# Kernel tuning notes

Hardware: AMD Instinct MI355X
Metric: run time of the kernel (lower is better)

The kernel has to match this reference:

```python
import jax, jax.numpy as jnp
import numpy as np


def setup_inputs() -> dict:
    key = jax.random.key(0)
    k1, k2, k3, k4, k5 = jax.random.split(key, 5)
    B, L, D = 8, 4096, 64
    return {
        "Q": jax.random.normal(k1, (B, L, D), dtype=jnp.float32),
        "K": jax.random.normal(k2, (B, L, D), dtype=jnp.float32),
        "V": jax.random.normal(k3, (B, L, D), dtype=jnp.float32),
        "sent_embed_slice": jax.random.normal(k4, (B, D), dtype=jnp.float32),
        "proj": jax.random.normal(k5, (D, D), dtype=jnp.float32),  # fixed phi projection (M, d)
        "qkv_size": 64,
        "masked": 1,
    }


def _phi(X, proj, M):
    # X: (B, L, d). Original applies phi per timestep slice x = X[:, t, :] of shape (B, d)
    # phi(x) = (1/sqrt(M)) * exp(-0.5 * ||x||_F) * exp(proj @ x), Frobenius norm over the (B, d) slice.
    logits = jnp.einsum("bld,md->blm", X, proj)            # (B, L, M)
    scale = jnp.exp(-0.5 * jnp.sqrt(jnp.sum(X * X, axis=(0, 2))))  # per-timestep scalar, (L,)
    return jnp.exp(logits) * scale[None, :, None] / jnp.sqrt(jnp.asarray(M, jnp.float32))


def reference(Q, K, V, sent_embed_slice, proj, qkv_size, masked):
    M = qkv_size
    phi_q = _phi(Q, proj, M)  # (B, L, M)
    phi_k = _phi(K, proj, M)  # (B, L, M)
    if masked:
        # causal running sums: KV_t = sum_{j<=t} phi_k_j outer V_j ; N_t = sum_{j<=t} phi_k_j
        KV = jnp.cumsum(phi_k[:, :, :, None] * V[:, :, None, :], axis=1)  # (B, L, M, D)
        Nc = jnp.cumsum(phi_k, axis=1)                                    # (B, L, M)
        num = jnp.einsum("blm,blmd->bld", phi_q, KV)
        r = jnp.einsum("blm,blm->bl", phi_q, Nc)
        return num / (r + jnp.sign(r) * 1e-6)[:, :, None]
    else:
        KV = jnp.einsum("blm,bld->bmd", phi_k, V)     # (B, M, D)
        Ns = jnp.sum(phi_k, axis=1)                    # (B, M); broadcast over D like torch norm_sum
        num = jnp.einsum("blm,bmd->bld", phi_q, KV)
        r = jnp.einsum("blm,bm->bl", phi_q, Ns)
        return num / r[:, :, None]
```

## Files before the change

kernel.cpp:

```cpp
#include <hip/hip_runtime.h>
#include <math.h>

#define BB 8
#define LL 4096
#define DD 64
#define SS 64
#define NCHUNK 64
#define STATE 4160

typedef __attribute__((ext_vector_type(8))) short s16x8;
typedef __attribute__((ext_vector_type(8))) unsigned short u16x8;
typedef __attribute__((ext_vector_type(4))) float f32x4;

#define MFMA(a, b, c) __builtin_amdgcn_mfma_f32_16x16x32_bf16((a), (b), (c), 0, 0, 0)

static __device__ __forceinline__ unsigned short f2bf(float x) {
  unsigned int u = __builtin_bit_cast(unsigned int, x);
  u += 0x7FFFu + ((u >> 16) & 1u);
  return (unsigned short)(u >> 16);
}
static __device__ __forceinline__ float bf2f(unsigned short h) {
  unsigned int u = ((unsigned int)h) << 16;
  return __builtin_bit_cast(float, u);
}

static __device__ __forceinline__ s16x8 ld_frag(const unsigned short* base, int row0, int ks) {
  const int lane = threadIdx.x & 63;
  const int r = row0 + (lane & 15);
  const int idx = r * 64 + ((ks * 32 + ((lane & 48) >> 1)) ^ ((r & 7) << 3));
  return *(const s16x8*)(base + idx);
}

static __device__ __forceinline__ void stage_hl(unsigned short* __restrict__ Sh,
                                                unsigned short* __restrict__ Sl,
                                                const float* __restrict__ src, int tid) {
#pragma unroll
  for (int it = 0; it < 2; ++it) {
    const int g = tid + it * 256;
    const int row = g >> 3;
    const int c0 = (g & 7) * 8;
    const float4 x0 = *(const float4*)(src + row * 64 + c0);
    const float4 x1 = *(const float4*)(src + row * 64 + c0 + 4);
    const float xs[8] = {x0.x, x0.y, x0.z, x0.w, x1.x, x1.y, x1.z, x1.w};
    u16x8 h, l;
#pragma unroll
    for (int k = 0; k < 8; ++k) {
      const unsigned short hh = f2bf(xs[k]);
      h[k] = hh;
      l[k] = f2bf(xs[k] - bf2f(hh));
    }
    const int idx = row * 64 + (c0 ^ ((row & 7) << 3));
    *(u16x8*)(Sh + idx) = h;
    *(u16x8*)(Sl + idx) = l;
  }
}

static __device__ __forceinline__ void stage_vfull(float* __restrict__ F, const float* __restrict__ src,
                                                   int tid) {
#pragma unroll
  for (int it = 0; it < 4; ++it) {
    const int g = tid + it * 256;
    const int row = g >> 4;
    const int col = (g & 15) * 4;
    *(float4*)(F + row * 64 + col) = *(const float4*)(src + row * 64 + col);
  }
}

static __device__ __forceinline__ void stage_img(unsigned short* __restrict__ S,
                                                 const unsigned short* __restrict__ src, int tid) {
#pragma unroll
  for (int it = 0; it < 2; ++it) {
    const int g = tid + it * 256;
    const int row = g >> 3;
    const int c0 = (g & 7) * 8;
    *(u16x8*)(S + row * 64 + (c0 ^ ((row & 7) << 3))) = *(const u16x8*)(src + row * 64 + c0);
  }
}

static __device__ __forceinline__ void vtrans_half(unsigned short* __restrict__ Gh,
                                                   unsigned short* __restrict__ Hl,
                                                   const float* __restrict__ F, int tid, int half) {
  const int d = tid & 63;
  const int tb = (tid >> 6) * 8;
  float v[8];
#pragma unroll
  for (int k = 0; k < 8; ++k) v[k] = F[(tb + k) * 64 + d];
  u16x8 hh, ll;
#pragma unroll
  for (int k = 0; k < 8; ++k) {
    const unsigned short h = f2bf(v[k]);
    hh[k] = h;
    ll[k] = f2bf(v[k] - bf2f(h));
  }
  const int idx = d * 64 + ((half * 32 + tb) ^ ((d & 7) << 3));
  *(u16x8*)(Gh + idx) = hh;
  *(u16x8*)(Hl + idx) = ll;
}

static __device__ __forceinline__ void logits3(const unsigned short* Ah_, const unsigned short* Al_,
                                               const unsigned short* Bh_, const unsigned short* Bl_,
                                               int w, f32x4 acc[4]) {
  s16x8 ah[2], al[2];
#pragma unroll
  for (int ks = 0; ks < 2; ++ks) {
    ah[ks] = ld_frag(Ah_, w * 16, ks);
    al[ks] = ld_frag(Al_, w * 16, ks);
  }
#pragma unroll
  for (int ct = 0; ct < 4; ++ct) {
#pragma unroll
    for (int ks = 0; ks < 2; ++ks) {
      const s16x8 bh = ld_frag(Bh_, ct * 16, ks);
      const s16x8 bl = ld_frag(Bl_, ct * 16, ks);
      acc[ct] = MFMA(ah[ks], bh, acc[ct]);
      acc[ct] = MFMA(ah[ks], bl, acc[ct]);
      acc[ct] = MFMA(al[ks], bh, acc[ct]);
    }
  }
}

static __device__ __forceinline__ void phi_store_row(unsigned short* dst, const f32x4* acc,
                                                     const float* sc, int w) {
  const int lane = threadIdx.x & 63;
#pragma unroll
  for (int ri = 0; ri < 4; ++ri) {
    const int t = w * 16 + ((lane & 48) >> 2) + ri;
#pragma unroll
    for (int ct = 0; ct < 4; ++ct) {
      const int m = ct * 16 + (lane & 15);
      dst[t * 64 + (m ^ ((t & 7) << 3))] = f2bf(__expf(acc[ct][ri]) * sc[ri]);
    }
  }
}

static __device__ __forceinline__ void phi_store_col_and_g(unsigned short* dstc,
                                                           unsigned short* __restrict__ gdst,
                                                           const f32x4* acc, const float* sc, int w) {
  const int lane = threadIdx.x & 63;
#pragma unroll
  for (int ri = 0; ri < 4; ++ri) {
    const int t = w * 16 + ((lane & 48) >> 2) + ri;
#pragma unroll
    for (int ct = 0; ct < 4; ++ct) {
      const int m = ct * 16 + (lane & 15);
      const unsigned short ph = f2bf(__expf(acc[ct][ri]) * sc[ri]);
      dstc[m * 64 + (t ^ ((m & 7) << 3))] = ph;
      gdst[t * 64 + m] = ph;
    }
  }
}

__global__ __launch_bounds__(256) void k_scales(const float* __restrict__ Q,
                                                const float* __restrict__ K,
                                                float* __restrict__ ws) {
  const int t = blockIdx.x * 4 + (threadIdx.x >> 6);
  const int lane = threadIdx.x & 63;
  const int b = lane >> 3;
  const int d0 = (lane & 7) * 8;
  const size_t base = (size_t)b * (LL * DD) + (size_t)t * DD + d0;
  float sq = 0.f, sk = 0.f;
#pragma unroll
  for (int k = 0; k < 8; ++k) {
    const float q = Q[base + k]; sq += q * q;
    const float kk = K[base + k]; sk += kk * kk;
  }
#pragma unroll
  for (int off = 32; off; off >>= 1) {
    sq += __shfl_xor(sq, off);
    sk += __shfl_xor(sk, off);
  }
  if (lane == 0) {
    ws[t]      = expf(-0.5f * sqrtf(sq));
    ws[LL + t] = expf(-0.5f * sqrtf(sk));
  }
}

__global__ __launch_bounds__(256) void k_chunk_sums(const float* __restrict__ Kg,
                                                    const float* __restrict__ Vg,
                                                    const float* __restrict__ proj,
                                                    const float* __restrict__ ws,
                                                    float* __restrict__ states,
                                                    unsigned short* __restrict__ phiKg) {
  __shared__ unsigned short A_[4096], B_[4096];
  __shared__ unsigned short C_[4096], D_[4096];
  __shared__ unsigned short E_[4096];
  __shared__ unsigned short G_[4096], H_[4096];
  __shared__ float F[4096];
  const int tid = threadIdx.x;
  const int lane = tid & 63;
  const int w = tid >> 6;
  const int bc = blockIdx.x;
  const int b = bc >> 6;
  const int c = bc & (NCHUNK - 1);
  const int t0 = c * SS;
  const size_t tileBase = ((size_t)b * LL + t0) * DD;
  float* stc = states + ((size_t)b * NCHUNK + c) * (size_t)STATE;
  unsigned short* pkT = phiKg + (size_t)bc * 4096;

  stage_hl(A_, B_, proj, tid);
  stage_hl(C_, D_, Kg + tileBase, tid);
  stage_vfull(F, Vg + tileBase, tid);
  float sck[4];
#pragma unroll
  for (int ri = 0; ri < 4; ++ri) {
    const int trow = w * 16 + ((lane & 48) >> 2) + ri;
    sck[ri] = ws[LL + t0 + trow] * 0.125f;
  }
  __syncthreads();

  {
    f32x4 acc[4] = {};
    logits3(C_, D_, A_, B_, w, acc);
    phi_store_col_and_g(E_, pkT, acc, sck, w);
  }
  vtrans_half(G_, H_, F, tid, 0);
  vtrans_half(G_, H_, F + 32 * 64, tid, 1);
  __syncthreads();

  {
    const int m = tid >> 2, q = tid & 3;
    float s = 0.f;
#pragma unroll
    for (int p = 0; p < 2; ++p) {
      const int tt = q * 16 + p * 8;
      const u16x8 vv = *(const u16x8*)(E_ + m * 64 + (tt ^ ((m & 7) << 3)));
#pragma unroll
      for (int i = 0; i < 8; ++i) s += bf2f(vv[i]);
    }
    s += __shfl_xor(s, 1);
    s += __shfl_xor(s, 2);
    if (q == 0) stc[4096 + m] = s;
  }
  {
    s16x8 avh[2], avl[2];
#pragma unroll
    for (int ks = 0; ks < 2; ++ks) {
      avh[ks] = ld_frag(G_, w * 16, ks);
      avl[ks] = ld_frag(H_, w * 16, ks);
    }
    f32x4 acc[4] = {};
#pragma unroll
    for (int ct = 0; ct < 4; ++ct)
#pragma unroll
      for (int ks = 0; ks < 2; ++ks) {
        const s16x8 bp = ld_frag(E_, ct * 16, ks);
        acc[ct] = MFMA(avh[ks], bp, acc[ct]);
        acc[ct] = MFMA(avl[ks], bp, acc[ct]);
      }
#pragma unroll
    for (int ri = 0; ri < 4; ++ri) {
      const int d = w * 16 + ((lane & 48) >> 2) + ri;
#pragma unroll
      for (int ct = 0; ct < 4; ++ct) {
        stc[d * 64 + ct * 16 + (lane & 15)] = acc[ct][ri];
      }
    }
  }
}

__global__ __launch_bounds__(256) void k_prefix1(const float* __restrict__ states,
                                                 float* __restrict__ tmp) {
  const int e = blockIdx.x * 256 + threadIdx.x;
  if (e >= BB * 8 * STATE) return;
  const int b = e / (8 * STATE);
  const int r = e % (8 * STATE);
  const int g = r / STATE;
  const int el = r % STATE;
  const float* p = states + ((size_t)b * NCHUNK + g * 8) * STATE + el;
  float s = 0.f;
#pragma unroll
  for (int i = 0; i < 8; ++i) s += p[(size_t)i * STATE];
  tmp[((size_t)b * 8 + g) * STATE + el] = s;
}

__global__ __launch_bounds__(256) void k_prefix2(float* __restrict__ states,
                                                 const float* __restrict__ tmp) {
  const int e = blockIdx.x * 256 + threadIdx.x;
  if (e >= BB * 8 * STATE) return;
  const int b = e / (8 * STATE);
  const int r = e % (8 * STATE);
  const int g = r / STATE;
  const int el = r % STATE;
  float run = 0.f;
  for (int g2 = 0; g2 < g; ++g2) run += tmp[((size_t)b * 8 + g2) * STATE + el];
  float* p = states + ((size_t)b * NCHUNK + g * 8) * STATE + el;
#pragma unroll
  for (int i = 0; i < 8; ++i) {
    const float v = p[(size_t)i * STATE];
    p[(size_t)i * STATE] = run;
    run += v;
  }
}

__global__ __launch_bounds__(256) void k_out(const float* __restrict__ Qg,
                                             const float* __restrict__ Vg,
                                             const float* __restrict__ proj,
                                             const unsigned short* __restrict__ phiKg,
                                             const float* __restrict__ ws,
                                             const float* __restrict__ states,
                                             float* __restrict__ out) {
  __shared__ unsigned short A_[4096], B_[4096];
  __shared__ unsigned short C_[4096];
  __shared__ unsigned short D_[4096];
  __shared__ unsigned short PK[4096];
  __shared__ unsigned short KV0[4096], KV1[4096];
  __shared__ float F[4096];
  const int tid = threadIdx.x;
  const int lane = tid & 63;
  const int w = tid >> 6;
  const int bc = blockIdx.x;
  const int b = bc >> 6;
  const int c = bc & (NCHUNK - 1);
  const int t0 = c * SS;
  const size_t tileBase = ((size_t)b * LL + t0) * DD;
  const float* st = states + ((size_t)b * NCHUNK + c) * (size_t)STATE;
  const unsigned short* pkT = phiKg + (size_t)bc * 4096;

  stage_hl(A_, B_, proj, tid);
  stage_hl(C_, D_, Qg + tileBase, tid);
  stage_img(PK, pkT, tid);
  stage_hl(KV0, KV1, st, tid);
  stage_vfull(F, Vg + tileBase, tid);
  float scq[4];
#pragma unroll
  for (int ri = 0; ri < 4; ++ri) {
    const int trow = w * 16 + ((lane & 48) >> 2) + ri;
    scq[ri] = ws[t0 + trow] * 0.125f;
  }
  __syncthreads();

  s16x8 aq[2];
  {
    f32x4 acc[4] = {};
    logits3(C_, D_, A_, B_, w, acc);
    phi_store_row(C_, acc, scq, w);
#pragma unroll
    for (int ks = 0; ks < 2; ++ks) aq[ks] = ld_frag(C_, w * 16, ks);
  }
  __syncthreads();

  vtrans_half(A_, B_, F, tid, 0);
  vtrans_half(A_, B_, F + 32 * 64, tid, 1);

  float rsI[4];
  {
    f32x4 accA[4] = {};
#pragma unroll
    for (int ct = 0; ct < 4; ++ct)
#pragma unroll
      for (int ks = 0; ks < 2; ++ks)
        accA[ct] = MFMA(aq[ks], ld_frag(PK, ct * 16, ks), accA[ct]);
#pragma unroll
    for (int ri = 0; ri < 4; ++ri) {
      const int t = w * 16 + ((lane & 48) >> 2) + ri;
      float part = 0.f;
#pragma unroll
      for (int ct = 0; ct < 4; ++ct) {
        const int j = ct * 16 + (lane & 15);
        const float a = (j <= t) ? accA[ct][ri] : 0.f;
        const unsigned short ah = f2bf(a);
        part += bf2f(ah);
        D_[t * 64 + (j ^ ((t & 7) << 3))] = ah;
      }
#pragma unroll
      for (int off = 1; off < 16; off <<= 1) part += __shfl_xor(part, off);
      rsI[ri] = part;
    }
  }
  __syncthreads();

  {
    s16x8 aA[2];
#pragma unroll
    for (int ks = 0; ks < 2; ++ks) aA[ks] = ld_frag(D_, w * 16, ks);
    f32x4 acc[4] = {};
#pragma unroll
    for (int ct = 0; ct < 4; ++ct) {
#pragma unroll
      for (int ks = 0; ks < 2; ++ks) {
        acc[ct] = MFMA(aA[ks], ld_frag(A_, ct * 16, ks), acc[ct]);
        acc[ct] = MFMA(aA[ks], ld_frag(B_, ct * 16, ks), acc[ct]);
        acc[ct] = MFMA(aq[ks], ld_frag(KV0, ct * 16, ks), acc[ct]);
        acc[ct] = MFMA(aq[ks], ld_frag(KV1, ct * 16, ks), acc[ct]);
      }
    }
    float rsp = 0.f;
    const float* Np = st + 4096;
#pragma unroll
    for (int ks = 0; ks < 2; ++ks) {
      const int m0 = ks * 32 + ((lane & 48) >> 1);
      const float4 n0 = *(const float4*)(Np + m0);
      const float4 n1 = *(const float4*)(Np + m0 + 4);
      const float nn[8] = {n0.x, n0.y, n0.z, n0.w, n1.x, n1.y, n1.z, n1.w};
#pragma unroll
      for (int i = 0; i < 8; ++i) rsp += bf2f((unsigned short)aq[ks][i]) * nn[i];
    }
    rsp += __shfl_xor(rsp, 16);
    rsp += __shfl_xor(rsp, 32);
#pragma unroll
    for (int ri = 0; ri < 4; ++ri) {
      const float r = rsI[ri] + __shfl(rsp, ((lane & 48) >> 2) + ri);
      const float inv = 1.f / (r + copysignf(1e-6f, r));
      const int t = w * 16 + ((lane & 48) >> 2) + ri;
#pragma unroll
      for (int ct = 0; ct < 4; ++ct) {
        out[tileBase + t * 64 + ct * 16 + (lane & 15)] = acc[ct][ri] * inv;
      }
    }
  }
}

extern "C" void kernel_launch(void* const* d_in, const int* in_sizes, int n_in,
                              void* d_out, int out_size, void* d_ws, size_t ws_size,
                              hipStream_t stream) {
  (void)in_sizes; (void)n_in; (void)out_size; (void)ws_size;
  const float* Q    = (const float*)d_in[0];
  const float* K    = (const float*)d_in[1];
  const float* V    = (const float*)d_in[2];
  const float* proj = (const float*)d_in[4];
  float* out = (float*)d_out;
  float* ws  = (float*)d_ws;
  float* states = ws + 2 * LL;
  const size_t statesFloats = (size_t)BB * NCHUNK * STATE;
  float* tmp = states + statesFloats;
  const size_t tmpFloats = (size_t)BB * 8 * STATE;
  unsigned short* phiKg = (unsigned short*)(tmp + tmpFloats);

  hipLaunchKernelGGL(k_scales, dim3(LL / 4), dim3(256), 0, stream, Q, K, ws);
  hipLaunchKernelGGL(k_chunk_sums, dim3(BB * NCHUNK), dim3(256), 0, stream,
                     K, V, proj, ws, states, phiKg);
  hipLaunchKernelGGL(k_prefix1, dim3((BB * 8 * STATE + 255) / 256), dim3(256), 0, stream, states, tmp);
  hipLaunchKernelGGL(k_prefix2, dim3((BB * 8 * STATE + 255) / 256), dim3(256), 0, stream, states, tmp);
  hipLaunchKernelGGL(k_out, dim3(BB * NCHUNK), dim3(256), 0, stream,
                     Q, V, proj, phiKg, ws, states, out);
}
```

Before: 34.54 us.

## Fuse prefix-scan second pass into output kernel via group offsets

Replaces the two-pass chunk prefix scan with a single kernel that writes exclusive group-level prefix sums. Each output block adds up to seven chunk states from its own group on the fly, then splits the result into bf16 hi/lo and writes it into LDS. This removes one kernel launch and the full read-modify-write of the states array. In exchange, k_out reads more global memory and its per-block load time varies with chunk position. The scales kernel also switches to float4 vector loads.

```diff
diff --git a/kernel.cpp b/kernel.cpp
--- a/kernel.cpp
+++ b/kernel.cpp
@@ -158,12 +158,14 @@
   const int b = lane >> 3;
   const int d0 = (lane & 7) * 8;
   const size_t base = (size_t)b * (LL * DD) + (size_t)t * DD + d0;
-  float sq = 0.f, sk = 0.f;
-#pragma unroll
-  for (int k = 0; k < 8; ++k) {
-    const float q = Q[base + k]; sq += q * q;
-    const float kk = K[base + k]; sk += kk * kk;
-  }
+  const float4 q0 = *(const float4*)(Q + base);
+  const float4 q1 = *(const float4*)(Q + base + 4);
+  const float4 k0 = *(const float4*)(K + base);
+  const float4 k1 = *(const float4*)(K + base + 4);
+  float sq = q0.x * q0.x + q0.y * q0.y + q0.z * q0.z + q0.w * q0.w +
+             q1.x * q1.x + q1.y * q1.y + q1.z * q1.z + q1.w * q1.w;
+  float sk = k0.x * k0.x + k0.y * k0.y + k0.z * k0.z + k0.w * k0.w +
+             k1.x * k1.x + k1.y * k1.y + k1.z * k1.z + k1.w * k1.w;
 #pragma unroll
   for (int off = 32; off; off >>= 1) {
     sq += __shfl_xor(sq, off);
@@ -258,37 +260,21 @@
   }
 }
 
-__global__ __launch_bounds__(256) void k_prefix1(const float* __restrict__ states,
-                                                 float* __restrict__ tmp) {
+__global__ __launch_bounds__(256) void k_groups(const float* __restrict__ states,
+                                                float* __restrict__ tmp) {
   const int e = blockIdx.x * 256 + threadIdx.x;
-  if (e >= BB * 8 * STATE) return;
-  const int b = e / (8 * STATE);
-  const int r = e % (8 * STATE);
-  const int g = r / STATE;
-  const int el = r % STATE;
-  const float* p = states + ((size_t)b * NCHUNK + g * 8) * STATE + el;
-  float s = 0.f;
-#pragma unroll
-  for (int i = 0; i < 8; ++i) s += p[(size_t)i * STATE];
-  tmp[((size_t)b * 8 + g) * STATE + el] = s;
-}
-
-__global__ __launch_bounds__(256) void k_prefix2(float* __restrict__ states,
-                                                 const float* __restrict__ tmp) {
-  const int e = blockIdx.x * 256 + threadIdx.x;
-  if (e >= BB * 8 * STATE) return;
-  const int b = e / (8 * STATE);
-  const int r = e % (8 * STATE);
-  const int g = r / STATE;
-  const int el = r % STATE;
+  if (e >= BB * STATE) return;
+  const int b = e / STATE;
+  const int el = e % STATE;
+  const float* p = states + (size_t)b * NCHUNK * STATE + el;
   float run = 0.f;
-  for (int g2 = 0; g2 < g; ++g2) run += tmp[((size_t)b * 8 + g2) * STATE + el];
-  float* p = states + ((size_t)b * NCHUNK + g * 8) * STATE + el;
-#pragma unroll
-  for (int i = 0; i < 8; ++i) {
-    const float v = p[(size_t)i * STATE];
-    p[(size_t)i * STATE] = run;
-    run += v;
+#pragma unroll
+  for (int g = 0; g < 8; ++g) {
+    tmp[((size_t)b * 8 + g) * STATE + el] = run;
+    float s = 0.f;
+#pragma unroll
+    for (int i = 0; i < 8; ++i) s += p[(size_t)(g * 8 + i) * STATE];
+    run += s;
   }
 }
 
@@ -298,6 +284,7 @@
                                              const unsigned short* __restrict__ phiKg,
                                              const float* __restrict__ ws,
                                              const float* __restrict__ states,
+                                             const float* __restrict__ tmp,
                                              float* __restrict__ out) {
   __shared__ unsigned short A_[4096], B_[4096];
   __shared__ unsigned short C_[4096];
@@ -305,22 +292,59 @@
   __shared__ unsigned short PK[4096];
   __shared__ unsigned short KV0[4096], KV1[4096];
   __shared__ float F[4096];
+  __shared__ float NP[64];
   const int tid = threadIdx.x;
   const int lane = tid & 63;
   const int w = tid >> 6;
   const int bc = blockIdx.x;
   const int b = bc >> 6;
   const int c = bc & (NCHUNK - 1);
+  const int g = c >> 3;
   const int t0 = c * SS;
   const size_t tileBase = ((size_t)b * LL + t0) * DD;
-  const float* st = states + ((size_t)b * NCHUNK + c) * (size_t)STATE;
+  const float* tgp = tmp + ((size_t)b * 8 + g) * STATE;
+  const float* stb = states + (size_t)b * NCHUNK * STATE;
   const unsigned short* pkT = phiKg + (size_t)bc * 4096;
+  const int ccnt = c - g * 8;
 
   stage_hl(A_, B_, proj, tid);
   stage_hl(C_, D_, Qg + tileBase, tid);
   stage_img(PK, pkT, tid);
-  stage_hl(KV0, KV1, st, tid);
   stage_vfull(F, Vg + tileBase, tid);
+
+#pragma unroll
+  for (int it = 0; it < 2; ++it) {
+    const int gg = tid + it * 256;
+    const int row = gg >> 3;
+    const int c0 = (gg & 7) * 8;
+    const int off = row * 64 + c0;
+    float4 a0 = *(const float4*)(tgp + off);
+    float4 a1 = *(const float4*)(tgp + off + 4);
+    for (int cc = 0; cc < ccnt; ++cc) {
+      const float* sp = stb + (size_t)(g * 8 + cc) * STATE + off;
+      const float4 s0 = *(const float4*)(sp);
+      const float4 s1 = *(const float4*)(sp + 4);
+      a0.x += s0.x; a0.y += s0.y; a0.z += s0.z; a0.w += s0.w;
+      a1.x += s1.x; a1.y += s1.y; a1.z += s1.z; a1.w += s1.w;
+    }
+    const float xs[8] = {a0.x, a0.y, a0.z, a0.w, a1.x, a1.y, a1.z, a1.w};
+    u16x8 h, l;
+#pragma unroll
+    for (int k = 0; k < 8; ++k) {
+      const unsigned short hh = f2bf(xs[k]);
+      h[k] = hh;
+      l[k] = f2bf(xs[k] - bf2f(hh));
+    }
+    const int idx = row * 64 + (c0 ^ ((row & 7) << 3));
+    *(u16x8*)(KV0 + idx) = h;
+    *(u16x8*)(KV1 + idx) = l;
+  }
+  if (tid < 64) {
+    float np = tgp[4096 + tid];
+    for (int cc = 0; cc < ccnt; ++cc) np += stb[(size_t)(g * 8 + cc) * STATE + 4096 + tid];
+    NP[tid] = np;
+  }
+
   float scq[4];
 #pragma unroll
   for (int ri = 0; ri < 4; ++ri) {
@@ -385,12 +409,11 @@
       }
     }
     float rsp = 0.f;
-    const float* Np = st + 4096;
 #pragma unroll
     for (int ks = 0; ks < 2; ++ks) {
       const int m0 = ks * 32 + ((lane & 48) >> 1);
-      const float4 n0 = *(const float4*)(Np + m0);
-      const float4 n1 = *(const float4*)(Np + m0 + 4);
+      const float4 n0 = *(const float4*)(NP + m0);
+      const float4 n1 = *(const float4*)(NP + m0 + 4);
       const float nn[8] = {n0.x, n0.y, n0.z, n0.w, n1.x, n1.y, n1.z, n1.w};
 #pragma unroll
       for (int i = 0; i < 8; ++i) rsp += bf2f((unsigned short)aq[ks][i]) * nn[i];
@@ -429,8 +452,7 @@
   hipLaunchKernelGGL(k_scales, dim3(LL / 4), dim3(256), 0, stream, Q, K, ws);
   hipLaunchKernelGGL(k_chunk_sums, dim3(BB * NCHUNK), dim3(256), 0, stream,
                      K, V, proj, ws, states, phiKg);
-  hipLaunchKernelGGL(k_prefix1, dim3((BB * 8 * STATE + 255) / 256), dim3(256), 0, stream, states, tmp);
-  hipLaunchKernelGGL(k_prefix2, dim3((BB * 8 * STATE + 255) / 256), dim3(256), 0, stream, states, tmp);
+  hipLaunchKernelGGL(k_groups, dim3((BB * STATE + 255) / 256), dim3(256), 0, stream, states, tmp);
   hipLaunchKernelGGL(k_out, dim3(BB * NCHUNK), dim3(256), 0, stream,
-                     Q, V, proj, phiKg, ws, states, out);
-}
+                     Q, V, proj, phiKg, ws, states, tmp, out);
+}
```

Result: slower. 38.62 us (+11.8%).

## Read V directly from global in transpose, coalesce phiK stores, vectorize scale loads

Applied to the files above, without the earlier changes.

Both chunk kernels drop the fp32 V staging tile in shared memory. Each thread now reads its 8 V elements for the transpose straight from global memory, one column per thread, which coalesces across lanes. The chunk-sums kernel also writes phi_K to a swizzled shared row buffer and then copies it to global with 16-byte vector stores, replacing scattered 2-byte global writes. The scales kernel switches to float4 loads. Together these cut LDS use, which may allow more blocks per CU, and remove uncoalesced writes, at the cost of more strided global reads for V.

```diff
diff --git a/kernel.cpp b/kernel.cpp
--- a/kernel.cpp
+++ b/kernel.cpp
@@ -55,17 +55,6 @@
   }
 }
 
-static __device__ __forceinline__ void stage_vfull(float* __restrict__ F, const float* __restrict__ src,
-                                                   int tid) {
-#pragma unroll
-  for (int it = 0; it < 4; ++it) {
-    const int g = tid + it * 256;
-    const int row = g >> 4;
-    const int col = (g & 15) * 4;
-    *(float4*)(F + row * 64 + col) = *(const float4*)(src + row * 64 + col);
-  }
-}
-
 static __device__ __forceinline__ void stage_img(unsigned short* __restrict__ S,
                                                  const unsigned short* __restrict__ src, int tid) {
 #pragma unroll
@@ -77,14 +66,14 @@
   }
 }
 
-static __device__ __forceinline__ void vtrans_half(unsigned short* __restrict__ Gh,
-                                                   unsigned short* __restrict__ Hl,
-                                                   const float* __restrict__ F, int tid, int half) {
+static __device__ __forceinline__ void vtrans_half_g(unsigned short* __restrict__ Gh,
+                                                     unsigned short* __restrict__ Hl,
+                                                     const float* __restrict__ Vt, int tid, int half) {
   const int d = tid & 63;
   const int tb = (tid >> 6) * 8;
   float v[8];
 #pragma unroll
-  for (int k = 0; k < 8; ++k) v[k] = F[(tb + k) * 64 + d];
+  for (int k = 0; k < 8; ++k) v[k] = Vt[(half * 32 + tb + k) * 64 + d];
   u16x8 hh, ll;
 #pragma unroll
   for (int k = 0; k < 8; ++k) {
@@ -133,9 +122,8 @@
   }
 }
 
-static __device__ __forceinline__ void phi_store_col_and_g(unsigned short* dstc,
-                                                           unsigned short* __restrict__ gdst,
-                                                           const f32x4* acc, const float* sc, int w) {
+static __device__ __forceinline__ void phi_store_col(unsigned short* dst, const f32x4* acc,
+                                                     const float* sc, int w) {
   const int lane = threadIdx.x & 63;
 #pragma unroll
   for (int ri = 0; ri < 4; ++ri) {
@@ -143,9 +131,7 @@
 #pragma unroll
     for (int ct = 0; ct < 4; ++ct) {
       const int m = ct * 16 + (lane & 15);
-      const unsigned short ph = f2bf(__expf(acc[ct][ri]) * sc[ri]);
-      dstc[m * 64 + (t ^ ((m & 7) << 3))] = ph;
-      gdst[t * 64 + m] = ph;
+      dst[m * 64 + (t ^ ((m & 7) << 3))] = f2bf(__expf(acc[ct][ri]) * sc[ri]);
     }
   }
 }
@@ -158,12 +144,14 @@
   const int b = lane >> 3;
   const int d0 = (lane & 7) * 8;
   const size_t base = (size_t)b * (LL * DD) + (size_t)t * DD + d0;
-  float sq = 0.f, sk = 0.f;
-#pragma unroll
-  for (int k = 0; k < 8; ++k) {
-    const float q = Q[base + k]; sq += q * q;
-    const float kk = K[base + k]; sk += kk * kk;
-  }
+  const float4 q0 = *(const float4*)(Q + base);
+  const float4 q1 = *(const float4*)(Q + base + 4);
+  const float4 k0 = *(const float4*)(K + base);
+  const float4 k1 = *(const float4*)(K + base + 4);
+  float sq = q0.x * q0.x + q0.y * q0.y + q0.z * q0.z + q0.w * q0.w +
+             q1.x * q1.x + q1.y * q1.y + q1.z * q1.z + q1.w * q1.w;
+  float sk = k0.x * k0.x + k0.y * k0.y + k0.z * k0.z + k0.w * k0.w +
+             k1.x * k1.x + k1.y * k1.y + k1.z * k1.z + k1.w * k1.w;
 #pragma unroll
   for (int off = 32; off; off >>= 1) {
     sq += __shfl_xor(sq, off);
@@ -185,7 +173,7 @@
   __shared__ unsigned short C_[4096], D_[4096];
   __shared__ unsigned short E_[4096];
   __shared__ unsigned short G_[4096], H_[4096];
-  __shared__ float F[4096];
+  __shared__ unsigned short R_[4096];
   const int tid = threadIdx.x;
   const int lane = tid & 63;
   const int w = tid >> 6;
@@ -199,7 +187,6 @@
 
   stage_hl(A_, B_, proj, tid);
   stage_hl(C_, D_, Kg + tileBase, tid);
-  stage_vfull(F, Vg + tileBase, tid);
   float sck[4];
 #pragma unroll
   for (int ri = 0; ri < 4; ++ri) {
@@ -211,12 +198,23 @@
   {
     f32x4 acc[4] = {};
     logits3(C_, D_, A_, B_, w, acc);
-    phi_store_col_and_g(E_, pkT, acc, sck, w);
-  }
-  vtrans_half(G_, H_, F, tid, 0);
-  vtrans_half(G_, H_, F + 32 * 64, tid, 1);
+    phi_store_col(E_, acc, sck, w);
+    phi_store_row(R_, acc, sck, w);
+  }
+  vtrans_half_g(G_, H_, Vg + tileBase, tid, 0);
+  vtrans_half_g(G_, H_, Vg + tileBase, tid, 1);
   __syncthreads();
 
+  {
+    const int r0 = tid >> 3;
+    const int c0 = (tid & 7) * 8;
+#pragma unroll
+    for (int it = 0; it < 2; ++it) {
+      const int r = r0 + it * 32;
+      const int sidx = r * 64 + (c0 ^ ((r & 7) << 3));
+      *(u16x8*)(pkT + r * 64 + c0) = *(const u16x8*)(R_ + sidx);
+    }
+  }
   {
     const int m = tid >> 2, q = tid & 3;
     float s = 0.f;
@@ -304,7 +302,6 @@
   __shared__ unsigned short D_[4096];
   __shared__ unsigned short PK[4096];
   __shared__ unsigned short KV0[4096], KV1[4096];
-  __shared__ float F[4096];
   const int tid = threadIdx.x;
   const int lane = tid & 63;
   const int w = tid >> 6;
@@ -320,7 +317,6 @@
   stage_hl(C_, D_, Qg + tileBase, tid);
   stage_img(PK, pkT, tid);
   stage_hl(KV0, KV1, st, tid);
-  stage_vfull(F, Vg + tileBase, tid);
   float scq[4];
 #pragma unroll
   for (int ri = 0; ri < 4; ++ri) {
@@ -339,8 +335,8 @@
   }
   __syncthreads();
 
-  vtrans_half(A_, B_, F, tid, 0);
-  vtrans_half(A_, B_, F + 32 * 64, tid, 1);
+  vtrans_half_g(A_, B_, Vg + tileBase, tid, 0);
+  vtrans_half_g(A_, B_, Vg + tileBase, tid, 1);
 
   float rsI[4];
   {
```

New measurement: 34.11 us (median of 3 runs). About the same (-1.2%).
